# Optimization experiments

Measured on AMD Instinct MI355X. Metric: run time of the kernel, lower is better.

## Reference

```python
import math
import jax, jax.numpy as jnp
import numpy as np

N, E, D, B, S, H = 16384, 196608, 256, 256, 64, 8
DH = D // H
BN_INV = 1.0 / math.sqrt(1.0 + 1e-5)  # eval-mode BN: mean=0, var=1, eps=1e-5
LOG2 = math.log(2.0)


def _mlp(x, w1, b1, w2, b2):
    # Linear -> SiLU -> Linear
    return jax.nn.silu(x @ w1 + b1) @ w2 + b2


def _bn(x, g, b):
    # BatchNorm1d in eval mode with running_mean=0, running_var=1
    return x * (BN_INV * g) + b


def _graph_ln(x, g, b):
    # pyg LayerNorm(mode='graph') called with batch=None: normalize over all nodes+features
    mu = jnp.mean(x)
    xc = x - mu
    var = jnp.mean(xc * xc)
    return xc * jax.lax.rsqrt(var + 1e-5) * g + b


def _forward(x, edge_index, edge_attr,
             node_w1, node_b1, node_w2, node_b2,
             c_w1, c_b1, c_w2, c_b2,
             bn_e_g, bn_e_b, bn_h_g, bn_h_b,
             n1l_g, n1l_b, n1a_g, n1a_b, n2_g, n2_b,
             wq, bq, wk, bk, wv, bv, wo, bo,
             aff_w1, aff_b1, aff_w2, aff_b2,
             fn_g, fn_b, fc_w1, fc_b1, fc_w2, fc_b2):
    row, col = edge_index[0], edge_index[1]

    # ---- PotNetConvGate local branch ----
    # A, B, V, U MLPs (all take node features) computed with stacked weights [4,D,D]
    hid = jax.nn.silu(jnp.einsum('nd,kdf->knf', x, node_w1) + node_b1[:, None, :])
    node_out = jnp.einsum('knf,kfg->kng', hid, node_w2) + node_b2[:, None, :]
    h_A, h_B, h_V, h_U = node_out[0], node_out[1], node_out[2], node_out[3]
    e_C = _mlp(edge_attr, c_w1, c_b1, c_w2, c_b2)  # [E,D]

    score = jax.nn.relu(_bn(h_A[row] + h_B[col] + e_C, bn_e_g, bn_e_b))  # [E,D]
    e_new = edge_attr + score

    # pyg softmax over edges grouped by destination node (col), per channel
    m = jax.ops.segment_max(e_new, col, num_segments=N)        # [N,D]
    ex = jnp.exp(e_new - m[col])
    s = jax.ops.segment_sum(ex, col, num_segments=N)           # [N,D]
    gated = ex / (s[col] + 1e-16)

    msg = gated * (h_V[col] + e_new)
    aggr = jax.ops.segment_sum(msg, col, num_segments=N)       # [N,D]
    h_local = jax.nn.silu(x + _bn(h_U + aggr, bn_h_g, bn_h_b))
    # e_out = silu(e_new + edge_attr)  # edge output, not used downstream for node output
    h_local = _bn(h_local, n1l_g, n1l_b)  # norm1_local

    # ---- global Transformer branch (equal-size graphs -> dense reshape, full mask) ----
    hd = x.reshape(B, S, D)
    q = (hd @ wq + bq).reshape(B, S, H, DH).transpose(0, 2, 1, 3)
    k = (hd @ wk + bk).reshape(B, S, H, DH).transpose(0, 2, 1, 3)
    v = (hd @ wv + bv).reshape(B, S, H, DH).transpose(0, 2, 1, 3)
    att = jax.nn.softmax(jnp.einsum('bhqd,bhkd->bhqk', q, k) / math.sqrt(DH), axis=-1)
    o = jnp.einsum('bhqk,bhkd->bhqd', att, v).transpose(0, 2, 1, 3).reshape(B, S, D)
    h_attn = (o @ wo + bo).reshape(N, D)

    h_attn = _bn(h_attn + x, n1a_g, n1a_b)  # norm1_attn
    t = jax.nn.gelu(h_attn @ aff_w1 + aff_b1, approximate=False) @ aff_w2 + aff_b2
    h_attn = _graph_ln(t + x, fn_g, fn_b)   # feed_norm

    # ---- fuse branches (mean over stacked outputs) ----
    h_new = (h_local + h_attn) * 0.5

    # ---- _ff_block: fc = Linear -> ShiftedSoftplus -> Linear ----
    ssp = jax.nn.softplus(h_new @ fc_w1 + fc_b1) - LOG2
    out = ssp @ fc_w2 + fc_b2
    return _bn(out + h_new, n2_g, n2_b)  # norm2


def setup_inputs():
    key = jax.random.key(0)
    ks = iter(jax.random.split(key, 64))
    sc = 1.0 / math.sqrt(D)
    def w(shape):
        return jax.random.normal(next(ks), shape, jnp.float32) * sc
    z = lambda *s: jnp.zeros(s, jnp.float32)
    o = lambda *s: jnp.ones(s, jnp.float32)
    return {
        'x': jax.random.normal(next(ks), (N, D), jnp.float32),
        'edge_index': jax.random.randint(next(ks), (2, E), 0, N, jnp.int32),
        'edge_attr': jax.random.normal(next(ks), (E, D), jnp.float32),
        'node_w1': w((4, D, D)), 'node_b1': z(4, D),
        'node_w2': w((4, D, D)), 'node_b2': z(4, D),
        'c_w1': w((D, D)), 'c_b1': z(D), 'c_w2': w((D, D)), 'c_b2': z(D),
        'bn_e_g': o(D), 'bn_e_b': z(D), 'bn_h_g': o(D), 'bn_h_b': z(D),
        'n1l_g': o(D), 'n1l_b': z(D), 'n1a_g': o(D), 'n1a_b': z(D),
        'n2_g': o(D), 'n2_b': z(D),
        'wq': w((D, D)), 'bq': z(D), 'wk': w((D, D)), 'bk': z(D),
        'wv': w((D, D)), 'bv': z(D), 'wo': w((D, D)), 'bo': z(D),
        'aff_w1': w((D, 2 * D)), 'aff_b1': z(2 * D),
        'aff_w2': w((2 * D, D)), 'aff_b2': z(D),
        'fn_g': o(D), 'fn_b': z(D),
        'fc_w1': w((D, 2 * D)), 'fc_b1': z(2 * D),
        'fc_w2': w((2 * D, D)), 'fc_b2': z(D),
    }


def reference(x, edge_index, edge_attr,
              node_w1, node_b1, node_w2, node_b2,
              c_w1, c_b1, c_w2, c_b2,
              bn_e_g, bn_e_b, bn_h_g, bn_h_b,
              n1l_g, n1l_b, n1a_g, n1a_b, n2_g, n2_b,
              wq, bq, wk, bk, wv, bv, wo, bo,
              aff_w1, aff_b1, aff_w2, aff_b2,
              fn_g, fn_b, fc_w1, fc_b1, fc_w2, fc_b2):
    return _forward(x, edge_index, edge_attr,
                    node_w1, node_b1, node_w2, node_b2,
                    c_w1, c_b1, c_w2, c_b2,
                    bn_e_g, bn_e_b, bn_h_g, bn_h_b,
                    n1l_g, n1l_b, n1a_g, n1a_b, n2_g, n2_b,
                    wq, bq, wk, bk, wv, bv, wo, bo,
                    aff_w1, aff_b1, aff_w2, aff_b2,
                    fn_g, fn_b, fc_w1, fc_b1, fc_w2, fc_b2)
```

## Files before the change

### kernel.cpp

```cpp
#include <hip/hip_runtime.h>
#include <hip/hip_bf16.h>
#include <stdint.h>

#define NN 16384
#define NE 196608
#define DD 256
#define ND 4194304
#define BNINV 0.9999950000374997f
#define LOG2F_ 0.6931471805599453f

typedef __attribute__((ext_vector_type(8))) short short8v;
typedef __attribute__((ext_vector_type(4))) float float4v;

__device__ __forceinline__ float b2f(__hip_bfloat16 v) { return __bfloat162float(v); }
__device__ __forceinline__ __hip_bfloat16 f2b(float v) { return __float2bfloat16(v); }

__device__ __forceinline__ void gl_lds16(const __hip_bfloat16* g, __hip_bfloat16* l) {
  __builtin_amdgcn_global_load_lds((const __attribute__((address_space(1))) void*)g,
                                   (__attribute__((address_space(3))) void*)l, 16, 0, 0);
}

#define VMW5 asm volatile("s_waitcnt vmcnt(5)" ::: "memory")
#define VMW4 asm volatile("s_waitcnt vmcnt(4)" ::: "memory")
#define VMW0 asm volatile("s_waitcnt vmcnt(0)" ::: "memory")
#define LKW0 asm volatile("s_waitcnt lgkmcnt(0)" ::: "memory")
#define SB __builtin_amdgcn_s_barrier()
#define SCB __builtin_amdgcn_sched_barrier(0)

__device__ __forceinline__ float rdf(const void* p, size_t i, int fl) {
  return fl ? b2f(((const __hip_bfloat16*)p)[i]) : ((const float*)p)[i];
}

__device__ __forceinline__ short8v cvt8(float4v f0, float4v f1) {
  short8v s;
#pragma unroll
  for (int i = 0; i < 4; ++i) {
    __hip_bfloat16 h0 = f2b(f0[i]), h1 = f2b(f1[i]);
    s[i] = *(short*)&h0;
    s[4 + i] = *(short*)&h1;
  }
  return s;
}

#define OFF_WT    0ul
#define OFF_PB    2883584ul
#define OFF_XB    2899968ul
#define OFF_HN    11288576ul
#define OFF_HL    44843008ul
#define OFF_EN    162283520ul
#define OFF_QKV   262946816ul
#define OFF_O     313278464ul
#define OFF_HATTN 321667072ul
#define OFF_HIDN  330055680ul
#define OFF_U     346832896ul
#define OFF_HNEW  363610112ul
#define OFF_HNEWB 380387328ul
#define OFF_TAIL  388775936ul
#define OFF_EB    390070272ul

#define PB_NB1   0
#define PB_NB2   1024
#define PB_CB1   2048
#define PB_CB2   2304
#define PB_QKVB  2560
#define PB_BO    3328
#define PB_AB1   3584
#define PB_AB2   4096
#define PB_FB1   4352
#define PB_FB2   4864
#define PB_BNEG  5120
#define PB_BNEB  5376
#define PB_BNHG  5632
#define PB_BNHB  5888
#define PB_N1LG  6144
#define PB_N1LB  6400
#define PB_N1AG  6656
#define PB_N1AB  6912
#define PB_N2G   7168
#define PB_N2B   7424
#define PB_FNG   7680
#define PB_FNB   7936

__global__ void probe_kernel(const uint32_t* bneg_raw, int* flag) {
  if (threadIdx.x == 0 && blockIdx.x == 0)
    *flag = (bneg_raw[0] == 0x3F803F80u) ? 1 : 0;
}

__global__ void canon_e(const float* __restrict__ e, __hip_bfloat16* __restrict__ EB,
                        const int* __restrict__ flagp) {
  if (*flagp) return;
  const size_t i = ((size_t)blockIdx.x * 256 + threadIdx.x) * 8;
  const float4v f0 = *(const float4v*)(e + i);
  const float4v f1 = *(const float4v*)(e + i + 4);
  *(short8v*)((short*)EB + i) = cvt8(f0, f1);
}

struct PJobs {
  const void* src[24];
  int off[24];
  int len[24];
};

__global__ void canon_params(PJobs jb, __hip_bfloat16* PB, const int* flagp) {
  const int fl = *flagp;
  const int j = blockIdx.x;
  const void* src = jb.src[j];
  const int off = jb.off[j], len = jb.len[j];
  for (int i = threadIdx.x; i < len; i += 256) PB[off + i] = f2b(rdf(src, i, fl));
}

__global__ void canon_x(const void* x, __hip_bfloat16* XB, const int* flagp) {
  const int fl = *flagp;
  const size_t i = (size_t)blockIdx.x * 256 + threadIdx.x;
  XB[i] = f2b(rdf(x, i, fl));
}

struct TJobsF {
  const void* src[18];
  __hip_bfloat16* dst[18];
  int R[18];
  int C[18];
  int RB[18];
};

__global__ void transpose_rb(TJobsF jb, const int* flagp) {
  __shared__ __hip_bfloat16 tile[32][33];
  const int fl = *flagp;
  const int j = blockIdx.z;
  const int R = jb.R[j], C = jb.C[j], RB = jb.RB[j];
  const int c0 = blockIdx.x * 32, r0 = blockIdx.y * 32;
  if (c0 >= C || r0 >= R) return;
  const void* src = jb.src[j];
  __hip_bfloat16* dst = jb.dst[j];
  const int tx = threadIdx.x, ty = threadIdx.y;
#pragma unroll
  for (int i = 0; i < 4; ++i)
    tile[ty + i * 8][tx] = f2b(rdf(src, (size_t)(RB + r0 + ty + i * 8) * C + c0 + tx, fl));
  __syncthreads();
#pragma unroll
  for (int i = 0; i < 4; ++i)
    dst[(long)(c0 + ty + i * 8) * R + r0 + tx] = tile[tx][ty + i * 8];
}

__global__ void prep_kernel(int* counts, double* stats) {
  const int i = blockIdx.x * blockDim.x + threadIdx.x;
  if (i < NN) counts[i] = 0;
  if (i == 0) counts[NN] = 0;
  if (i < 2) stats[i] = 0.0;
}

template <int ACT, int RES, int BNM, int OUTBF, int DUALOUT>
__global__ __launch_bounds__(256) void gemm_bt(
    const void* __restrict__ Avp, const __hip_bfloat16* __restrict__ Wt,
    const __hip_bfloat16* __restrict__ bias, const void* __restrict__ Res,
    const __hip_bfloat16* __restrict__ bng, const __hip_bfloat16* __restrict__ bnb,
    void* __restrict__ Cout, const int* __restrict__ flagp,
    int M, int N, int K, long boff, long az, long wz, long bz, long cz) {
  __shared__ __align__(16) __hip_bfloat16 sA[2][128 * 32];
  __shared__ __align__(16) __hip_bfloat16 sB[2][128 * 32];
  const int fl = DUALOUT ? *flagp : 1;
  const int z = blockIdx.z;
  const long aoff = boff + (long)z * az;
  const __hip_bfloat16* Ab = (const __hip_bfloat16*)Avp + aoff;
  Wt += (long)z * wz;
  bias += (long)z * bz;
  const long coff = (long)z * cz;
  const int tid = threadIdx.x;
  const int lane = tid & 63;
  const int wid = tid >> 6;
  const int wm = wid >> 1, wn = wid & 1;
  const int l16 = lane & 15, lq = lane >> 4;
  const long am0 = (long)blockIdx.y * 128;
  const long bn0 = (long)blockIdx.x * 128;

  float4v acc[4][4] = {};

  const int nK = K >> 5;
  auto STG = [&](int t, int b) {
#pragma unroll
    for (int r = 0; r < 2; ++r) {
      const int c = tid + r * 256;
      gl_lds16(Ab + (am0 + (c >> 2)) * (long)K + (long)t * 32 + (c & 3) * 8, sA[b] + c * 8);
      gl_lds16(Wt + (bn0 + (c >> 2)) * (long)K + (long)t * 32 + (c & 3) * 8, sB[b] + c * 8);
    }
  };

  STG(0, 0);
  STG(1, 1);
  VMW4;
  SB;

  for (int kb = 0; kb < nK; ++kb) {
    const int cur = kb & 1;
    const short* pA = (const short*)sA[cur];
    const short* pB = (const short*)sB[cur];
    short8v af[4], bv_[4];
#pragma unroll
    for (int mi = 0; mi < 4; ++mi)
      af[mi] = *(const short8v*)(pA + (wm * 64 + mi * 16 + l16) * 32 + lq * 8);
#pragma unroll
    for (int ni = 0; ni < 4; ++ni)
      bv_[ni] = *(const short8v*)(pB + (wn * 64 + ni * 16 + l16) * 32 + lq * 8);
    LKW0;
    SCB;
    SB;
    if (kb + 2 < nK) STG(kb + 2, cur);
#pragma unroll
    for (int mi = 0; mi < 4; ++mi)
#pragma unroll
      for (int ni = 0; ni < 4; ++ni)
        acc[mi][ni] =
            __builtin_amdgcn_mfma_f32_16x16x32_bf16(af[mi], bv_[ni], acc[mi][ni], 0, 0, 0);
    if (kb + 1 < nK) {
      if (kb + 2 < nK) VMW4; else VMW0;
      SB;
    }
  }

  const __hip_bfloat16* Rb = (const __hip_bfloat16*)Res;
  const float* Rf = (const float*)Res;
#pragma unroll
  for (int mi = 0; mi < 4; ++mi) {
#pragma unroll
    for (int ni = 0; ni < 4; ++ni) {
#pragma unroll
      for (int r = 0; r < 4; ++r) {
        const long row = am0 + wm * 64 + mi * 16 + lq * 4 + r;
        const long col = bn0 + wn * 64 + ni * 16 + l16;
        float v = acc[mi][ni][r] + b2f(bias[col]);
        if (ACT == 1) v = v / (1.f + __expf(-v));
        else if (ACT == 2) v = 0.5f * v * (1.f + erff(v * 0.7071067811865476f));
        else if (ACT == 3) v = (v > 15.f ? v : log1pf(__expf(v))) - LOG2F_;
        if (RES == 1) v += b2f(Rb[row * N + col]);
        else if (RES == 2) v += Rf[row * N + col];
        if (BNM) v = v * (BNINV * b2f(bng[col])) + b2f(bnb[col]);
        if (DUALOUT) {
          if (fl) ((__hip_bfloat16*)Cout)[coff + row * N + col] = f2b(v);
          else ((float*)Cout)[coff + row * N + col] = v;
        } else if (OUTBF) {
          ((__hip_bfloat16*)Cout)[coff + row * N + col] = f2b(v);
        } else {
          ((float*)Cout)[coff + row * N + col] = v;
        }
      }
    }
  }
}

template <int EPI>
__global__ __launch_bounds__(256) void mlp_fused(
    const __hip_bfloat16* __restrict__ Adef, const __hip_bfloat16* __restrict__ W1t,
    const __hip_bfloat16* __restrict__ b1, const __hip_bfloat16* __restrict__ W2t,
    const __hip_bfloat16* __restrict__ b2, __hip_bfloat16* __restrict__ Out,
    const int* __restrict__ ei, const void* __restrict__ eattr,
    const __hip_bfloat16* __restrict__ EB, const __hip_bfloat16* __restrict__ HA,
    __hip_bfloat16* __restrict__ EN, const __hip_bfloat16* __restrict__ PB,
    const int* __restrict__ perm, const int* __restrict__ flagp, long wz, long cz) {
  __shared__ __align__(16) __hip_bfloat16 sA[2][64 * 32];
  __shared__ __align__(16) __hip_bfloat16 sW[2][256 * 32];
  __shared__ __align__(16) __hip_bfloat16 sH[64 * 264];
  const int z = blockIdx.z;
  const __hip_bfloat16* Ab =
      (EPI == 1) ? ((*flagp) ? (const __hip_bfloat16*)eattr : EB) : Adef;
  W1t += (long)z * wz;
  W2t += (long)z * wz;
  b1 += z * 256;
  b2 += z * 256;
  const int tid = threadIdx.x;
  const int lane = tid & 63;
  const int wn = tid >> 6;
  const int l16 = lane & 15, lq = lane >> 4;
  const long m0 = (long)blockIdx.y * 64;

  auto STA = [&](int t, int b) {
    gl_lds16(Ab + (m0 + (tid >> 2)) * 256 + t * 32 + (tid & 3) * 8, sA[b] + tid * 8);
  };
  auto STW = [&](const __hip_bfloat16* W, int t, int b) {
#pragma unroll
    for (int r = 0; r < 4; ++r) {
      const int c = r * 256 + tid;
      gl_lds16(W + (c >> 2) * 256 + t * 32 + (c & 3) * 8, sW[b] + c * 8);
    }
  };

  float4v acc[4][4] = {};

  STA(0, 0); STW(W1t, 0, 0);
  STA(1, 1); STW(W1t, 1, 1);
  VMW5;
  SB;
  for (int kb = 0; kb < 8; ++kb) {
    const int cur = kb & 1;
    const short* pA = (const short*)sA[cur];
    const short* pW = (const short*)sW[cur];
    short8v af[4], bf_[4];
#pragma unroll
    for (int mi = 0; mi < 4; ++mi)
      af[mi] = *(const short8v*)(pA + (mi * 16 + l16) * 32 + lq * 8);
#pragma unroll
    for (int ni = 0; ni < 4; ++ni)
      bf_[ni] = *(const short8v*)(pW + (wn * 64 + ni * 16 + l16) * 32 + lq * 8);
    LKW0;
    SCB;
    SB;
    if (kb + 2 < 8) { STA(kb + 2, cur); STW(W1t, kb + 2, cur); }
#pragma unroll
    for (int mi = 0; mi < 4; ++mi)
#pragma unroll
      for (int ni = 0; ni < 4; ++ni)
        acc[mi][ni] =
            __builtin_amdgcn_mfma_f32_16x16x32_bf16(af[mi], bf_[ni], acc[mi][ni], 0, 0, 0);
    if (kb + 1 < 8) {
      if (kb + 2 < 8) VMW5; else VMW0;
      SB;
    }
  }

  {
    short* hp = (short*)sH;
#pragma unroll
    for (int mi = 0; mi < 4; ++mi)
#pragma unroll
      for (int ni = 0; ni < 4; ++ni)
#pragma unroll
        for (int r = 0; r < 4; ++r) {
          const int row = mi * 16 + lq * 4 + r;
          const int col = wn * 64 + ni * 16 + l16;
          float v = acc[mi][ni][r] + b2f(b1[col]);
          v = v / (1.f + __expf(-v));
          __hip_bfloat16 hb = f2b(v);
          hp[row * 264 + col] = *(short*)&hb;
          acc[mi][ni][r] = 0.f;
        }
  }
  STW(W2t, 0, 0);
  STW(W2t, 1, 1);
  LKW0;
  VMW4;
  SB;

  for (int kb = 0; kb < 8; ++kb) {
    const int cur = kb & 1;
    const short* pW = (const short*)sW[cur];
    short8v af[4], bf_[4];
#pragma unroll
    for (int mi = 0; mi < 4; ++mi)
      af[mi] = *(const short8v*)((const short*)sH + (mi * 16 + l16) * 264 + kb * 32 + lq * 8);
#pragma unroll
    for (int ni = 0; ni < 4; ++ni)
      bf_[ni] = *(const short8v*)(pW + (wn * 64 + ni * 16 + l16) * 32 + lq * 8);
    LKW0;
    SCB;
    SB;
    if (kb + 2 < 8) STW(W2t, kb + 2, cur);
#pragma unroll
    for (int mi = 0; mi < 4; ++mi)
#pragma unroll
      for (int ni = 0; ni < 4; ++ni)
        acc[mi][ni] =
            __builtin_amdgcn_mfma_f32_16x16x32_bf16(af[mi], bf_[ni], acc[mi][ni], 0, 0, 0);
    if (kb + 1 < 8) {
      if (kb + 2 < 8) VMW4; else VMW0;
      SB;
    }
  }

  if (EPI == 0) {
#pragma unroll
    for (int mi = 0; mi < 4; ++mi)
#pragma unroll
      for (int ni = 0; ni < 4; ++ni)
#pragma unroll
        for (int r = 0; r < 4; ++r) {
          const long row = m0 + mi * 16 + lq * 4 + r;
          const int col = wn * 64 + ni * 16 + l16;
          Out[(long)z * cz + row * 256 + col] = f2b(acc[mi][ni][r] + b2f(b2[col]));
        }
  } else {
    const __hip_bfloat16* HB = HA + (size_t)ND;
#pragma unroll
    for (int mi = 0; mi < 4; ++mi)
#pragma unroll
      for (int r = 0; r < 4; ++r) {
        const long ge = m0 + mi * 16 + lq * 4 + r;
        const int rr = ei[ge];
        const int cc = ei[NE + ge];
        const long pe = perm[ge];
#pragma unroll
        for (int ni = 0; ni < 4; ++ni) {
          const int col = wn * 64 + ni * 16 + l16;
          float v = acc[mi][ni][r] + b2f(b2[col]);
          v += b2f(HA[(size_t)rr * DD + col]) + b2f(HB[(size_t)cc * DD + col]);
          v = v * (BNINV * b2f(PB[PB_BNEG + col])) + b2f(PB[PB_BNEB + col]);
          v = fmaxf(v, 0.f);
          v += b2f(Ab[(size_t)ge * DD + col]);
          EN[(size_t)pe * DD + col] = f2b(v);
        }
      }
  }
}

__global__ void count_kernel(const int* __restrict__ ei, int* __restrict__ counts) {
  const int e = blockIdx.x * 256 + threadIdx.x;
  if (e < NE) atomicAdd(&counts[ei[NE + e]], 1);
}

__global__ __launch_bounds__(1024) void scan_kernel(int* __restrict__ counts,
                                                    int* __restrict__ cursor) {
  __shared__ int part[1024];
  const int t = threadIdx.x;
  const int base = t * 16;
  int ss = 0;
#pragma unroll
  for (int i = 0; i < 16; ++i) ss += counts[base + i];
  part[t] = ss;
  __syncthreads();
  for (int off = 1; off < 1024; off <<= 1) {
    int v = (t >= off) ? part[t - off] : 0;
    __syncthreads();
    part[t] += v;
    __syncthreads();
  }
  int run = part[t] - ss;
  for (int i = 0; i < 16; ++i) {
    const int cv = counts[base + i];
    counts[base + i] = run;
    cursor[base + i] = run;
    run += cv;
  }
  if (t == 1023) counts[NN] = run;
}

__global__ void scatter_kernel(const int* __restrict__ ei, int* __restrict__ cursor,
                               int* __restrict__ perm) {
  const int e = blockIdx.x * 256 + threadIdx.x;
  if (e < NE) {
    const int p = atomicAdd(&cursor[ei[NE + e]], 1);
    perm[e] = p;
  }
}

__global__ __launch_bounds__(256) void segment_kernel(
    const int* __restrict__ offs, const __hip_bfloat16* __restrict__ EN,
    const __hip_bfloat16* __restrict__ hV, const __hip_bfloat16* __restrict__ hU,
    const __hip_bfloat16* __restrict__ XB, const __hip_bfloat16* __restrict__ PB,
    float* __restrict__ hlocal) {
  const int n = blockIdx.x;
  const int d = threadIdx.x;
  const int beg = offs[n], end = offs[n + 1];
  float sa = 0.f, sb = 0.f;
  int p = beg;
  for (; p + 4 <= end; p += 4) {
    const float v0 = b2f(EN[(size_t)(p + 0) * DD + d]);
    const float v1 = b2f(EN[(size_t)(p + 1) * DD + d]);
    const float v2 = b2f(EN[(size_t)(p + 2) * DD + d]);
    const float v3 = b2f(EN[(size_t)(p + 3) * DD + d]);
    const float e0 = __expf(v0), e1 = __expf(v1), e2 = __expf(v2), e3 = __expf(v3);
    sa += (e0 + e1) + (e2 + e3);
    sb += (e0 * v0 + e1 * v1) + (e2 * v2 + e3 * v3);
  }
  for (; p < end; ++p) {
    const float v = b2f(EN[(size_t)p * DD + d]);
    const float e = __expf(v);
    sa += e;
    sb += e * v;
  }
  const float hv = b2f(hV[(size_t)n * DD + d]);
  const float ag = (hv * sa + sb) / (sa + 1e-16f);
  const float t1 =
      (b2f(hU[(size_t)n * DD + d]) + ag) * (BNINV * b2f(PB[PB_BNHG + d])) + b2f(PB[PB_BNHB + d]);
  float s1 = b2f(XB[(size_t)n * DD + d]) + t1;
  s1 = s1 / (1.f + __expf(-s1));
  s1 = s1 * (BNINV * b2f(PB[PB_N1LG + d])) + b2f(PB[PB_N1LB + d]);
  hlocal[(size_t)n * DD + d] = s1;
}

__global__ __launch_bounds__(256) void attn_kernel(const float* __restrict__ QKV,
                                                   __hip_bfloat16* __restrict__ O) {
  __shared__ float sq[64][33], sk[64][33], sv[64][33];
  __shared__ float sp[64][65];
  const int bh = blockIdx.x;
  const int b = bh >> 3, h = bh & 7;
  const int tid = threadIdx.x;
  const float* Q = QKV;
  const float* Kp = QKV + (size_t)ND;
  const float* Vp = QKV + 2 * (size_t)ND;
#pragma unroll
  for (int j = 0; j < 8; ++j) {
    const int idx = j * 256 + tid;
    const int s = idx >> 5, dh = idx & 31;
    const size_t ga = ((size_t)(b * 64 + s)) * DD + h * 32 + dh;
    sq[s][dh] = Q[ga];
    sk[s][dh] = Kp[ga];
    sv[s][dh] = Vp[ga];
  }
  __syncthreads();
  const int row = tid >> 2, l4 = tid & 3;
  float qr[32];
#pragma unroll
  for (int d = 0; d < 32; ++d) qr[d] = sq[row][d];
  float sc[16];
  float mx = -1e30f;
#pragma unroll
  for (int jj = 0; jj < 16; ++jj) {
    const int j = l4 * 16 + jj;
    float dot = 0.f;
#pragma unroll
    for (int d = 0; d < 32; ++d) dot += qr[d] * sk[j][d];
    dot *= 0.17677669529663687f;
    sc[jj] = dot;
    mx = fmaxf(mx, dot);
  }
  mx = fmaxf(mx, __shfl_xor(mx, 1));
  mx = fmaxf(mx, __shfl_xor(mx, 2));
  float se = 0.f;
#pragma unroll
  for (int jj = 0; jj < 16; ++jj) {
    sc[jj] = __expf(sc[jj] - mx);
    se += sc[jj];
  }
  se += __shfl_xor(se, 1);
  se += __shfl_xor(se, 2);
  const float inv = 1.f / se;
#pragma unroll
  for (int jj = 0; jj < 16; ++jj) sp[row][l4 * 16 + jj] = sc[jj] * inv;
  __syncthreads();
#pragma unroll
  for (int k8 = 0; k8 < 8; ++k8) {
    const int dh = l4 * 8 + k8;
    float acc = 0.f;
#pragma unroll
    for (int j = 0; j < 64; ++j) acc += sp[row][j] * sv[j][dh];
    O[((size_t)(b * 64 + row)) * DD + h * 32 + dh] = f2b(acc);
  }
}

__global__ __launch_bounds__(256) void stats_kernel(const float* __restrict__ U,
                                                    double* __restrict__ st) {
  double s = 0.0, s2 = 0.0;
  for (size_t i = (size_t)blockIdx.x * 256 + threadIdx.x; i < (size_t)ND;
       i += (size_t)gridDim.x * 256) {
    const double v = (double)U[i];
    s += v;
    s2 += v * v;
  }
  for (int o = 32; o > 0; o >>= 1) {
    s += __shfl_down(s, o);
    s2 += __shfl_down(s2, o);
  }
  __shared__ double wred[4][2];
  const int lane = threadIdx.x & 63, w = threadIdx.x >> 6;
  if (lane == 0) {
    wred[w][0] = s;
    wred[w][1] = s2;
  }
  __syncthreads();
  if (threadIdx.x == 0) {
    double a = 0, bb = 0;
    for (int i = 0; i < 4; ++i) {
      a += wred[i][0];
      bb += wred[i][1];
    }
    atomicAdd(&st[0], a);
    atomicAdd(&st[1], bb);
  }
}

__global__ void finalize_stats(double* st) {
  if (threadIdx.x == 0 && blockIdx.x == 0) {
    const double mu = st[0] / (double)ND;
    const double var = st[1] / (double)ND - mu * mu;
    float* f = (float*)(st + 2);
    f[0] = (float)mu;
    f[1] = (float)(1.0 / sqrt(var + 1e-5));
  }
}

__global__ void hnew_kernel(const float* __restrict__ U, const float* __restrict__ hlocal,
                            const double* __restrict__ st, const __hip_bfloat16* __restrict__ PB,
                            float* __restrict__ HNEW, __hip_bfloat16* __restrict__ HNEWB) {
  const size_t i = (size_t)blockIdx.x * 256 + threadIdx.x;
  const float* f = (const float*)(st + 2);
  const float mu = f[0], rs = f[1];
  const int d = (int)(i & 255);
  const float ha = (U[i] - mu) * rs * b2f(PB[PB_FNG + d]) + b2f(PB[PB_FNB + d]);
  const float hn = 0.5f * (hlocal[i] + ha);
  HNEW[i] = hn;
  HNEWB[i] = f2b(hn);
}

extern "C" void kernel_launch(void* const* d_in, const int* in_sizes, int n_in, void* d_out,
                              int out_size, void* d_ws, size_t ws_size, hipStream_t stream) {
  (void)in_sizes; (void)n_in; (void)out_size; (void)ws_size;
  const void* x = d_in[0];
  const int* ei = (const int*)d_in[1];
  const void* eattr = d_in[2];

  uint8_t* ws = (uint8_t*)d_ws;
  __hip_bfloat16* WT = (__hip_bfloat16*)(ws + OFF_WT);
  __hip_bfloat16* PB = (__hip_bfloat16*)(ws + OFF_PB);
  __hip_bfloat16* XB = (__hip_bfloat16*)(ws + OFF_XB);
  __hip_bfloat16* HN = (__hip_bfloat16*)(ws + OFF_HN);
  float* HL = (float*)(ws + OFF_HL);
  __hip_bfloat16* EN = (__hip_bfloat16*)(ws + OFF_EN);
  float* QKV = (float*)(ws + OFF_QKV);
  __hip_bfloat16* O = (__hip_bfloat16*)(ws + OFF_O);
  __hip_bfloat16* HATTN = (__hip_bfloat16*)(ws + OFF_HATTN);
  __hip_bfloat16* HIDN = (__hip_bfloat16*)(ws + OFF_HIDN);
  float* U = (float*)(ws + OFF_U);
  float* HNEW = (float*)(ws + OFF_HNEW);
  __hip_bfloat16* HNEWB = (__hip_bfloat16*)(ws + OFF_HNEWB);
  __hip_bfloat16* EBp = (__hip_bfloat16*)(ws + OFF_EB);
  uint8_t* tail = ws + OFF_TAIL;
  int* counts = (int*)tail;
  int* cursor = (int*)(tail + 66048ul);
  int* perm = (int*)(tail + 132096ul);
  double* stats = (double*)(tail + 918528ul);
  int* flag = (int*)(tail + 918592ul);

  probe_kernel<<<1, 64, 0, stream>>>((const uint32_t*)d_in[11], flag);

  canon_e<<<24576, 256, 0, stream>>>((const float*)eattr, EBp, flag);

  PJobs pj;
  {
    const int srcidx[24] = {4, 6, 8, 10, 22, 24, 26, 28, 30, 32, 36, 38,
                            11, 12, 13, 14, 15, 16, 17, 18, 19, 20, 33, 34};
    const int dstoff[24] = {PB_NB1, PB_NB2, PB_CB1, PB_CB2, PB_QKVB, PB_QKVB + 256,
                            PB_QKVB + 512, PB_BO, PB_AB1, PB_AB2, PB_FB1, PB_FB2,
                            PB_BNEG, PB_BNEB, PB_BNHG, PB_BNHB, PB_N1LG, PB_N1LB,
                            PB_N1AG, PB_N1AB, PB_N2G, PB_N2B, PB_FNG, PB_FNB};
    const int lens[24] = {1024, 1024, 256, 256, 256, 256, 256, 256, 512, 256, 512, 256,
                          256, 256, 256, 256, 256, 256, 256, 256, 256, 256, 256, 256};
    for (int i = 0; i < 24; ++i) {
      pj.src[i] = d_in[srcidx[i]];
      pj.off[i] = dstoff[i];
      pj.len[i] = lens[i];
    }
  }
  canon_params<<<24, 256, 0, stream>>>(pj, PB, flag);
  canon_x<<<NN, 256, 0, stream>>>(x, XB, flag);

  TJobsF jf;
  for (int j = 0; j < 4; ++j) {
    jf.src[j] = d_in[3]; jf.dst[j] = WT + j * 65536;
    jf.R[j] = 256; jf.C[j] = 256; jf.RB[j] = j * 256;
    jf.src[4 + j] = d_in[5]; jf.dst[4 + j] = WT + 262144 + j * 65536;
    jf.R[4 + j] = 256; jf.C[4 + j] = 256; jf.RB[4 + j] = j * 256;
  }
  {
    const int widx[10] = {7, 9, 21, 23, 25, 27, 29, 31, 35, 37};
    const long wdst[10] = {524288, 589824, 655360, 720896, 786432, 851968,
                           917504, 1048576, 1179648, 1310720};
    const int wR[10] = {256, 256, 256, 256, 256, 256, 256, 512, 256, 512};
    const int wC[10] = {256, 256, 256, 256, 256, 256, 512, 256, 512, 256};
    for (int j = 0; j < 10; ++j) {
      jf.src[8 + j] = d_in[widx[j]]; jf.dst[8 + j] = WT + wdst[j];
      jf.R[8 + j] = wR[j]; jf.C[8 + j] = wC[j]; jf.RB[8 + j] = 0;
    }
  }
  transpose_rb<<<dim3(16, 16, 18), dim3(32, 8), 0, stream>>>(jf, flag);

  prep_kernel<<<64, 256, 0, stream>>>(counts, stats);

  count_kernel<<<768, 256, 0, stream>>>(ei, counts);
  scan_kernel<<<1, 1024, 0, stream>>>(counts, cursor);
  scatter_kernel<<<768, 256, 0, stream>>>(ei, cursor, perm);

  mlp_fused<0><<<dim3(1, 256, 4), 256, 0, stream>>>(
      XB, WT, PB + PB_NB1, WT + 262144, PB + PB_NB2, HN,
      nullptr, nullptr, nullptr, nullptr, nullptr, PB, nullptr, flag, 65536, ND);

  mlp_fused<1><<<dim3(1, 3072, 1), 256, 0, stream>>>(
      nullptr, WT + 524288, PB + PB_CB1, WT + 589824, PB + PB_CB2, nullptr,
      ei, eattr, EBp, HN, EN, PB, perm, flag, 0, 0);

  segment_kernel<<<NN, 256, 0, stream>>>(counts, EN, HN + 2 * (size_t)ND,
                                         HN + 3 * (size_t)ND, XB, PB, HL);

  gemm_bt<0, 0, 0, 0, 0><<<dim3(2, 128, 3), 256, 0, stream>>>(
      XB, WT + 655360, PB + PB_QKVB, nullptr, nullptr, nullptr, QKV, flag,
      NN, DD, DD, 0, 0, 65536, 256, ND);
  attn_kernel<<<2048, 256, 0, stream>>>(QKV, O);
  gemm_bt<0, 1, 1, 1, 0><<<dim3(2, 128, 1), 256, 0, stream>>>(
      O, WT + 851968, PB + PB_BO, XB, PB + PB_N1AG, PB + PB_N1AB, HATTN, flag,
      NN, DD, DD, 0, 0, 0, 0, 0);

  gemm_bt<2, 0, 0, 1, 0><<<dim3(4, 128, 1), 256, 0, stream>>>(
      HATTN, WT + 917504, PB + PB_AB1, nullptr, nullptr, nullptr, HIDN, flag,
      NN, 512, DD, 0, 0, 0, 0, 0);
  gemm_bt<0, 1, 0, 0, 0><<<dim3(2, 128, 1), 256, 0, stream>>>(
      HIDN, WT + 1048576, PB + PB_AB2, XB, nullptr, nullptr, U, flag,
      NN, DD, 512, 0, 0, 0, 0, 0);

  stats_kernel<<<1024, 256, 0, stream>>>(U, stats);
  finalize_stats<<<1, 64, 0, stream>>>(stats);
  hnew_kernel<<<NN, 256, 0, stream>>>(U, HL, stats, PB, HNEW, HNEWB);

  gemm_bt<3, 0, 0, 1, 0><<<dim3(4, 128, 1), 256, 0, stream>>>(
      HNEWB, WT + 1179648, PB + PB_FB1, nullptr, nullptr, nullptr, HIDN, flag,
      NN, 512, DD, 0, 0, 0, 0, 0);
  gemm_bt<0, 2, 1, 1, 1><<<dim3(2, 128, 1), 256, 0, stream>>>(
      HIDN, WT + 1310720, PB + PB_FB2, HNEW, PB + PB_N2G, PB + PB_N2B, d_out, flag,
      NN, DD, 512, 0, 0, 0, 0, 0);
}
```

Baseline: 888.7 us.

## Fuse graph-LN stats into GEMM epilogue and vectorize edge-score epilogue via LDS

The sum and sum-of-squares needed for the graph LayerNorm are now accumulated in the epilogue of the second affine GEMM, with per-wave shuffle reductions and double atomics. This removes the separate stats kernel and its extra full read of U. The edge MLP epilogue now stages accumulators through LDS so each lane handles 4 contiguous channels per edge. Gathers of h_A, h_B, edge_attr and the permuted EN store become 4-wide vector accesses instead of scattered scalar ones. In exchange the kernel issues many more double atomics, one pair per wave, and adds LDS round trips and barriers.

```diff
diff --git a/kernel.cpp b/kernel.cpp
--- a/kernel.cpp
+++ b/kernel.cpp
@@ -10,10 +10,16 @@
 #define LOG2F_ 0.6931471805599453f
 
 typedef __attribute__((ext_vector_type(8))) short short8v;
+typedef __attribute__((ext_vector_type(4))) short short4v;
 typedef __attribute__((ext_vector_type(4))) float float4v;
 
 __device__ __forceinline__ float b2f(__hip_bfloat16 v) { return __bfloat162float(v); }
 __device__ __forceinline__ __hip_bfloat16 f2b(float v) { return __float2bfloat16(v); }
+__device__ __forceinline__ float bs2f(short s) {
+  __hip_bfloat16 h;
+  *(short*)&h = s;
+  return __bfloat162float(h);
+}
 
 __device__ __forceinline__ void gl_lds16(const __hip_bfloat16* g, __hip_bfloat16* l) {
   __builtin_amdgcn_global_load_lds((const __attribute__((address_space(1))) void*)g,
@@ -149,7 +155,7 @@
   if (i < 2) stats[i] = 0.0;
 }
 
-template <int ACT, int RES, int BNM, int OUTBF, int DUALOUT>
+template <int ACT, int RES, int BNM, int OUTBF, int DUALOUT, int STAT>
 __global__ __launch_bounds__(256) void gemm_bt(
     const void* __restrict__ Avp, const __hip_bfloat16* __restrict__ Wt,
     const __hip_bfloat16* __restrict__ bias, const void* __restrict__ Res,
@@ -219,6 +225,7 @@
 
   const __hip_bfloat16* Rb = (const __hip_bfloat16*)Res;
   const float* Rf = (const float*)Res;
+  double s = 0.0, s2 = 0.0;
 #pragma unroll
   for (int mi = 0; mi < 4; ++mi) {
 #pragma unroll
@@ -234,6 +241,10 @@
         if (RES == 1) v += b2f(Rb[row * N + col]);
         else if (RES == 2) v += Rf[row * N + col];
         if (BNM) v = v * (BNINV * b2f(bng[col])) + b2f(bnb[col]);
+        if (STAT) {
+          s += (double)v;
+          s2 += (double)v * (double)v;
+        }
         if (DUALOUT) {
           if (fl) ((__hip_bfloat16*)Cout)[coff + row * N + col] = f2b(v);
           else ((float*)Cout)[coff + row * N + col] = v;
@@ -243,6 +254,17 @@
           ((float*)Cout)[coff + row * N + col] = v;
         }
       }
+    }
+  }
+  if (STAT) {
+    for (int o = 32; o > 0; o >>= 1) {
+      s += __shfl_down(s, o);
+      s2 += __shfl_down(s2, o);
+    }
+    if (lane == 0) {
+      double* stp = (double*)bng;
+      atomicAdd(&stp[0], s);
+      atomicAdd(&stp[1], s2);
     }
   }
 }
@@ -260,8 +282,9 @@
   __shared__ __align__(16) __hip_bfloat16 sW[2][256 * 32];
   __shared__ __align__(16) __hip_bfloat16 sH[64 * 264];
   const int z = blockIdx.z;
+  const int fl = (EPI == 1) ? *flagp : 1;
   const __hip_bfloat16* Ab =
-      (EPI == 1) ? ((*flagp) ? (const __hip_bfloat16*)eattr : EB) : Adef;
+      (EPI == 1) ? (fl ? (const __hip_bfloat16*)eattr : EB) : Adef;
   W1t += (long)z * wz;
   W2t += (long)z * wz;
   b1 += z * 256;
@@ -377,26 +400,66 @@
           Out[(long)z * cz + row * 256 + col] = f2b(acc[mi][ni][r] + b2f(b2[col]));
         }
   } else {
+    float* sF = (float*)sH;
     const __hip_bfloat16* HB = HA + (size_t)ND;
-#pragma unroll
-    for (int mi = 0; mi < 4; ++mi)
-#pragma unroll
-      for (int r = 0; r < 4; ++r) {
-        const long ge = m0 + mi * 16 + lq * 4 + r;
+    const __hip_bfloat16* Eh = (const __hip_bfloat16*)eattr;
+    const float* Ef = (const float*)eattr;
+    const int c0 = lane * 4;
+    float ga[4], gb[4];
+#pragma unroll
+    for (int k = 0; k < 4; ++k) {
+      ga[k] = BNINV * b2f(PB[PB_BNEG + c0 + k]);
+      gb[k] = b2f(PB[PB_BNEB + c0 + k]);
+    }
+#pragma unroll
+    for (int p = 0; p < 2; ++p) {
+#pragma unroll
+      for (int mm = 0; mm < 2; ++mm) {
+        const int mi = p * 2 + mm;
+#pragma unroll
+        for (int ni = 0; ni < 4; ++ni)
+#pragma unroll
+          for (int r = 0; r < 4; ++r) {
+            const int rl = mm * 16 + lq * 4 + r;
+            const int col = wn * 64 + ni * 16 + l16;
+            sF[rl * 264 + col] = acc[mi][ni][r] + b2f(b2[col]);
+          }
+      }
+      __syncthreads();
+#pragma unroll
+      for (int j = 0; j < 8; ++j) {
+        const int rl = wn * 8 + j;
+        const long ge = m0 + p * 32 + rl;
         const int rr = ei[ge];
         const int cc = ei[NE + ge];
         const long pe = perm[ge];
-#pragma unroll
-        for (int ni = 0; ni < 4; ++ni) {
-          const int col = wn * 64 + ni * 16 + l16;
-          float v = acc[mi][ni][r] + b2f(b2[col]);
-          v += b2f(HA[(size_t)rr * DD + col]) + b2f(HB[(size_t)cc * DD + col]);
-          v = v * (BNINV * b2f(PB[PB_BNEG + col])) + b2f(PB[PB_BNEB + col]);
+        const short4v ha4 = *(const short4v*)(HA + (size_t)rr * DD + c0);
+        const short4v hb4 = *(const short4v*)(HB + (size_t)cc * DD + c0);
+        float ev[4];
+        if (fl) {
+          const short4v e4 = *(const short4v*)(Eh + (size_t)ge * DD + c0);
+#pragma unroll
+          for (int k = 0; k < 4; ++k) ev[k] = bs2f(e4[k]);
+        } else {
+          const float4v e4 = *(const float4v*)(Ef + (size_t)ge * DD + c0);
+#pragma unroll
+          for (int k = 0; k < 4; ++k) ev[k] = e4[k];
+        }
+        const float4v g4 = *(const float4v*)(sF + rl * 264 + c0);
+        short4v o;
+#pragma unroll
+        for (int k = 0; k < 4; ++k) {
+          float v = g4[k] + (bs2f(ha4[k]) + bs2f(hb4[k]));
+          v = v * ga[k] + gb[k];
           v = fmaxf(v, 0.f);
-          v += b2f(Ab[(size_t)ge * DD + col]);
-          EN[(size_t)pe * DD + col] = f2b(v);
+          v += ev[k];
+          __hip_bfloat16 ob = f2b(v);
+          o[k] = *(short*)&ob;
         }
+        *(short4v*)(EN + (size_t)pe * DD + c0) = o;
       }
+      if (p == 0) __syncthreads();
+    }
   }
 }
 
@@ -532,37 +595,6 @@
 #pragma unroll
     for (int j = 0; j < 64; ++j) acc += sp[row][j] * sv[j][dh];
     O[((size_t)(b * 64 + row)) * DD + h * 32 + dh] = f2b(acc);
-  }
-}
-
-__global__ __launch_bounds__(256) void stats_kernel(const float* __restrict__ U,
-                                                    double* __restrict__ st) {
-  double s = 0.0, s2 = 0.0;
-  for (size_t i = (size_t)blockIdx.x * 256 + threadIdx.x; i < (size_t)ND;
-       i += (size_t)gridDim.x * 256) {
-    const double v = (double)U[i];
-    s += v;
-    s2 += v * v;
-  }
-  for (int o = 32; o > 0; o >>= 1) {
-    s += __shfl_down(s, o);
-    s2 += __shfl_down(s2, o);
-  }
-  __shared__ double wred[4][2];
-  const int lane = threadIdx.x & 63, w = threadIdx.x >> 6;
-  if (lane == 0) {
-    wred[w][0] = s;
-    wred[w][1] = s2;
-  }
-  __syncthreads();
-  if (threadIdx.x == 0) {
-    double a = 0, bb = 0;
-    for (int i = 0; i < 4; ++i) {
-      a += wred[i][0];
-      bb += wred[i][1];
-    }
-    atomicAdd(&st[0], a);
-    atomicAdd(&st[1], bb);
   }
 }
 
@@ -678,29 +710,28 @@
   segment_kernel<<<NN, 256, 0, stream>>>(counts, EN, HN + 2 * (size_t)ND,
                                          HN + 3 * (size_t)ND, XB, PB, HL);
 
-  gemm_bt<0, 0, 0, 0, 0><<<dim3(2, 128, 3), 256, 0, stream>>>(
+  gemm_bt<0, 0, 0, 0, 0, 0><<<dim3(2, 128, 3), 256, 0, stream>>>(
       XB, WT + 655360, PB + PB_QKVB, nullptr, nullptr, nullptr, QKV, flag,
       NN, DD, DD, 0, 0, 65536, 256, ND);
   attn_kernel<<<2048, 256, 0, stream>>>(QKV, O);
-  gemm_bt<0, 1, 1, 1, 0><<<dim3(2, 128, 1), 256, 0, stream>>>(
+  gemm_bt<0, 1, 1, 1, 0, 0><<<dim3(2, 128, 1), 256, 0, stream>>>(
       O, WT + 851968, PB + PB_BO, XB, PB + PB_N1AG, PB + PB_N1AB, HATTN, flag,
       NN, DD, DD, 0, 0, 0, 0, 0);
 
-  gemm_bt<2, 0, 0, 1, 0><<<dim3(4, 128, 1), 256, 0, stream>>>(
+  gemm_bt<2, 0, 0, 1, 0, 0><<<dim3(4, 128, 1), 256, 0, stream>>>(
       HATTN, WT + 917504, PB + PB_AB1, nullptr, nullptr, nullptr, HIDN, flag,
       NN, 512, DD, 0, 0, 0, 0, 0);
-  gemm_bt<0, 1, 0, 0, 0><<<dim3(2, 128, 1), 256, 0, stream>>>(
-      HIDN, WT + 1048576, PB + PB_AB2, XB, nullptr, nullptr, U, flag,
+  gemm_bt<0, 1, 0, 0, 0, 1><<<dim3(2, 128, 1), 256, 0, stream>>>(
+      HIDN, WT + 1048576, PB + PB_AB2, XB, (const __hip_bfloat16*)stats, nullptr, U, flag,
       NN, DD, 512, 0, 0, 0, 0, 0);
 
-  stats_kernel<<<1024, 256, 0, stream>>>(U, stats);
   finalize_stats<<<1, 64, 0, stream>>>(stats);
   hnew_kernel<<<NN, 256, 0, stream>>>(U, HL, stats, PB, HNEW, HNEWB);
 
-  gemm_bt<3, 0, 0, 1, 0><<<dim3(4, 128, 1), 256, 0, stream>>>(
+  gemm_bt<3, 0, 0, 1, 0, 0><<<dim3(4, 128, 1), 256, 0, stream>>>(
       HNEWB, WT + 1179648, PB + PB_FB1, nullptr, nullptr, nullptr, HIDN, flag,
       NN, 512, DD, 0, 0, 0, 0, 0);
-  gemm_bt<0, 2, 1, 1, 1><<<dim3(2, 128, 1), 256, 0, stream>>>(
+  gemm_bt<0, 2, 1, 1, 1, 0><<<dim3(2, 128, 1), 256, 0, stream>>>(
       HIDN, WT + 1310720, PB + PB_FB2, HNEW, PB + PB_N2G, PB + PB_N2B, d_out, flag,
       NN, DD, 512, 0, 0, 0, 0, 0);
 }
```

Measured after the change: 944.4 us. 1.06x slower.
